# Optimization experiments

Hardware: AMD Instinct MI355X
Metric: run time of the kernel (lower is better)

Reference implementation:

```python
import jax, jax.numpy as jnp
import numpy as np

B = 4096
D = 64  # emb_dim, hardcoded in UserEmb/ItemEmb


def setup_inputs() -> dict:
    key = jax.random.key(0)
    ks = jax.random.split(key, 26)
    n = lambda k, shape, s=1.0: jax.random.normal(k, shape, dtype=jnp.float32) * s
    inp = {
        'user_emb': jax.random.randint(ks[0], (B, 4), 0, 6, dtype=jnp.int32),
        'item_emb': jax.random.randint(ks[1], (B, 10242), 0, 2, dtype=jnp.int32),
        'edge_emb': jnp.zeros((B,), dtype=jnp.int32),  # edges_emb has num_embeddings=1
        # UserEmb params
        'gender_tab': n(ks[2], (98, D)),
        'age_tab': n(ks[3], (7, D)),
        'occ_tab': n(ks[4], (21, D)),
        'area_tab': n(ks[5], (3402, D)),
        'user_W': n(ks[6], (4 * D, D), 0.05),  # stored [in,out]
        'user_b': n(ks[7], (D,), 0.05),
        # ItemEmb params
        'rate_tab': n(ks[8], (6, D)),
        'genre_W': n(ks[9], (25, D), 0.05),
        'director_W': n(ks[10], (2186, D), 0.02),
        'actor_W': n(ks[11], (8030, D), 0.01),
        'item_W': n(ks[12], (4 * D, D), 0.05),
        'item_b': n(ks[13], (D,), 0.05),
        # GLNFeat params (torch: randn * 0.5)
        'edges_tab': n(ks[14], (1, D)),
        'uu_w': n(ks[15], (D,), 0.5),
        'ui_w': n(ks[16], (D,), 0.5),
        'iu_w': n(ks[17], (D,), 0.5),
        'ii_w': n(ks[18], (D,), 0.5),
        'edge_W': n(ks[19], (D, D), 0.5),
        'uu_W1': n(ks[20], (D, D), 0.5),
        'ui_W1': n(ks[21], (D, D), 0.5),
        'iu_W1': n(ks[22], (D, D), 0.5),
        'ii_W1': n(ks[23], (D, D), 0.5),
    }
    return inp


def _lrelu(v):
    return jnp.where(v >= 0, v, 0.01 * v)  # nn.LeakyReLU default slope


def reference(user_emb, item_emb, edge_emb, gender_tab, age_tab, occ_tab, area_tab,
              user_W, user_b, rate_tab, genre_W, director_W, actor_W, item_W, item_b,
              edges_tab, uu_w, ui_w, iu_w, ii_w, edge_W, uu_W1, ui_W1, iu_W1, ii_W1):
    a = 0.12
    b = 0.12
    # UserEmb
    u_cat = jnp.concatenate([gender_tab[user_emb[:, 0]], age_tab[user_emb[:, 1]],
                             occ_tab[user_emb[:, 2]], area_tab[user_emb[:, 3]]], axis=1)
    x = (u_cat @ user_W + user_b) * a  # [B, D]
    # ItemEmb: multi-hot fields projected then mean-normalized by count
    genre = item_emb[:, 1:26].astype(jnp.float32)
    director = item_emb[:, 26:2212].astype(jnp.float32)
    actor = item_emb[:, 2212:10242].astype(jnp.float32)
    ge = (genre @ genre_W) / jnp.sum(genre, 1, keepdims=True)
    de = (director @ director_W) / jnp.sum(director, 1, keepdims=True)
    ae = (actor @ actor_W) / jnp.sum(actor, 1, keepdims=True)
    i_cat = jnp.concatenate([rate_tab[item_emb[:, 0]], ge, de, ae], axis=1)
    y = (i_cat @ item_W + item_b) * a  # [B, D]
    edge = edges_tab[edge_emb] * b  # [B, D]

    def outer_mm(u, v, M):
        # stop_gradient(outer(u, v) @ M) == u[:,None] * (v @ M), avoids [B,B]
        return jax.lax.stop_gradient(u[:, None] * (v @ M))

    xe = x * edge
    ye = y * edge
    x_xx = xe @ uu_w      # [B]
    x_xy_x = xe @ ui_w
    x_xy_y = ye @ ui_w
    t1 = outer_mm(x_xx, x_xx, x)
    t2 = outer_mm(x_xy_x, x_xy_y, y)
    x_buy = (_lrelu(t1 @ uu_W1) + _lrelu(t2 @ ui_W1)) / 2
    y_yy = ye @ ii_w
    y_yx_y = ye @ iu_w
    y_yx_x = xe @ iu_w
    t3 = outer_mm(y_yy, y_yy, y)
    t4 = outer_mm(y_yx_y, y_yx_x, x)
    y_buy = (_lrelu(t3 @ ii_W1) + _lrelu(t4 @ iu_W1)) / 2
    new = _lrelu(edge @ edge_W)
    return ((x_buy + x) / 2, (y_buy + y) / 2, (new + edge) / 2)
```

## Files before the change

### kernel.cpp

```cpp
#include <hip/hip_runtime.h>
#include <cstddef>

constexpr int BATCH = 4096;
constexpr int ITEM_COLS = 10242;

constexpr int R_GENDER = 0;
constexpr int R_AGE    = 98;
constexpr int R_OCC    = 105;
constexpr int R_AREA   = 126;
constexpr int R_RATE   = 3528;
constexpr int R_FU     = 3534;

__device__ const int CUM[10] = {0, 128, 1280, 2432, 3840, 5248, 6656, 8064, 9472, 10880};
__device__ const int DLT[9]  = {0, -104, -168, -224, -296, -368, -432, -504, -576};
__device__ const int LOG[9]  = {1, 130, 1287, 2436, 3846, 5256, 6659, 8069, 9479};
__device__ const int HIG[9]  = {26, 1223, 2380, 3774, 5184, 6595, 7997, 9407, 10818};
constexpr int FB2COLS = 10880;
constexpr int NSLICE  = 15;
__device__ const int TS_[16] = {0, 1, 7, 13, 19, 25, 31, 37, 43, 49, 55, 61, 67, 73, 79, 85};
__device__ const int TCH[85] = {
    0,
    1,1,1,1,1,1,1,1,1,
    2,2,2,2,2,2,2,2,2,
    3,3,3,3,3,3,3,3,3,3,3,
    4,4,4,4,4,4,4,4,4,4,4,
    5,5,5,5,5,5,5,5,5,5,5,
    6,6,6,6,6,6,6,6,6,6,6,
    7,7,7,7,7,7,7,7,7,7,7,
    8,8,8,8,8,8,8,8,8,8,8};

constexpr int NFUSEA = 884;
constexpr int NFUSET = FB2COLS / 64;

constexpr size_t OFF_FU  = 0;
constexpr size_t OFF_NEW = OFF_FU + (size_t)R_FU * 64;
constexpr size_t OFF_FBT = OFF_NEW + 64;
constexpr size_t OFF_X   = OFF_FBT + (size_t)64 * FB2COLS / 2;
constexpr size_t OFF_Y   = OFF_X + (size_t)BATCH * 64;
constexpr size_t OFF_P   = OFF_Y + (size_t)BATCH * 64;
constexpr size_t OFF_C   = OFF_P + (size_t)NSLICE * BATCH * 64;
constexpr size_t OFF_SP  = OFF_C + (size_t)NSLICE * BATCH;
constexpr size_t OFF_SC  = OFF_SP + 256ull * 256;

typedef __attribute__((ext_vector_type(8))) short bf16x8;
typedef __attribute__((ext_vector_type(4))) float f32x4;

__device__ __forceinline__ float lrelu(float v) { return v >= 0.0f ? v : 0.01f * v; }

__device__ __forceinline__ unsigned bf_rne_pair(float lo, float hi) {
    unsigned ul = __builtin_bit_cast(unsigned, lo);
    unsigned uh = __builtin_bit_cast(unsigned, hi);
    ul += 0x7fffu + ((ul >> 16) & 1u);
    uh += 0x7fffu + ((uh >> 16) & 1u);
    return (ul >> 16) | (uh & 0xffff0000u);
}

__global__ __launch_bounds__(256) void k_fuse(
        const float* __restrict__ gender_tab, const float* __restrict__ age_tab,
        const float* __restrict__ occ_tab, const float* __restrict__ area_tab,
        const float* __restrict__ user_W, const float* __restrict__ rate_tab,
        const float* __restrict__ item_W, const float* __restrict__ edges_tab,
        const float* __restrict__ edge_W, const float* __restrict__ genre_W,
        const float* __restrict__ director_W, const float* __restrict__ actor_W,
        float* __restrict__ Fu, float* __restrict__ NEWt, short* __restrict__ Fbt2) {
    const int t = threadIdx.x;
    const int n = t & 63;
    const int rb = __builtin_amdgcn_readfirstlane(t >> 6);
    __shared__ float T[64 * 65];
    const int blk = blockIdx.x;

    if (blk < NFUSEA) {
        int r = blk * 4 + rb;
        if (r > R_FU) return;
        if (r == R_FU) {
            float acc = 0.0f;
#pragma unroll
            for (int k = 0; k < 64; ++k)
                acc = fmaf(edges_tab[k] * 0.12f, edge_W[k * 64 + n], acc);
            NEWt[n] = lrelu(acc);
            return;
        }
        const float* src;
        const float* W;
        if (r < R_AGE)       { src = gender_tab + (size_t)r * 64;            W = user_W;            }
        else if (r < R_OCC)  { src = age_tab    + (size_t)(r - R_AGE) * 64;  W = user_W + 64 * 64;  }
        else if (r < R_AREA) { src = occ_tab    + (size_t)(r - R_OCC) * 64;  W = user_W + 128 * 64; }
        else if (r < R_RATE) { src = area_tab   + (size_t)(r - R_AREA) * 64; W = user_W + 192 * 64; }
        else                 { src = rate_tab   + (size_t)(r - R_RATE) * 64; W = item_W;            }
        float acc = 0.0f;
#pragma unroll
        for (int k = 0; k < 64; ++k)
            acc = fmaf(src[k], W[k * 64 + n], acc);
        Fu[(size_t)r * 64 + n] = acc;
        return;
    }

    const int g0 = (blk - NFUSEA) * 64;
    int ch = 0;
    while (g0 >= CUM[ch + 1]) ++ch;
    const int lo = LOG[ch], hi = HIG[ch], dl = DLT[ch];

    for (int rl = 0; rl < 16; ++rl) {
        int r = rl * 4 + rb;
        int g = g0 + r;
        float acc = 0.0f;
        if (g >= lo && g < hi) {
            int c = g + dl;
            const float* src;
            const float* W;
            if (c < 26)        { src = genre_W    + (size_t)(c - 1) * 64;    W = item_W + 64 * 64;  }
            else if (c < 2212) { src = director_W + (size_t)(c - 26) * 64;   W = item_W + 128 * 64; }
            else               { src = actor_W    + (size_t)(c - 2212) * 64; W = item_W + 192 * 64; }
#pragma unroll
            for (int k = 0; k < 64; ++k)
                acc = fmaf(src[k], W[k * 64 + n], acc);
        }
        T[r * 65 + n] = acc;
    }
    __syncthreads();
    int n2 = t >> 2, sg = t & 3;
    unsigned dw[8];
#pragma unroll
    for (int d = 0; d < 8; ++d)
        dw[d] = bf_rne_pair(T[(sg * 16 + 2 * d) * 65 + n2], T[(sg * 16 + 2 * d + 1) * 65 + n2]);
    uint4* dst = (uint4*)(Fbt2 + (size_t)n2 * FB2COLS + g0 + sg * 16);
    dst[0] = make_uint4(dw[0], dw[1], dw[2], dw[3]);
    dst[1] = make_uint4(dw[4], dw[5], dw[6], dw[7]);
}

__global__ __launch_bounds__(256) void k_item(const int* __restrict__ item,
                                              const short* __restrict__ Fbt2,
                                              float* __restrict__ P, float* __restrict__ C) {
    const int slc = blockIdx.y;
    const int kt0 = TS_[slc], kt1 = TS_[slc + 1];
    const int m0 = blockIdx.x * 64;
    const int t = threadIdx.x;
    const int lane = t & 63;
    const int w = __builtin_amdgcn_readfirstlane(t >> 6);
    const int q = lane >> 4, r16 = lane & 15;

    __shared__ short As[64 * 136];
    __shared__ short Bs[64 * 136];

    f32x4 acc[5];
#pragma unroll
    for (int s = 0; s < 5; ++s) acc[s] = (f32x4){0.f, 0.f, 0.f, 0.f};

    const short o = (r16 == 0) ? (short)0x3f80 : (short)0;
    const bf16x8 ones = {o, o, o, o, o, o, o, o};

    int2 av[16];
    uint4 bv[4];
    const int nB = t >> 2, pt = t & 3;
    const int* arow = item + (size_t)(m0 + w) * ITEM_COLS + 2 * lane;
    const short* brow = Fbt2 + (size_t)nB * FB2COLS;

    auto fetch = [&](int kt) {
        const int ch = TCH[kt];
        const int c0 = kt * 128 + DLT[ch];
        if (c0 + 128 <= ITEM_COLS) {
            const int* ap = arow + c0;
#pragma unroll
            for (int it = 0; it < 16; ++it)
                av[it] = *(const int2*)(ap + (size_t)it * 4 * ITEM_COLS);
        } else {
            const bool ok = (c0 + 2 * lane) <= (ITEM_COLS - 2);
            const int ccl = ok ? (c0 + 2 * lane) : (ITEM_COLS - 2);
            const int* ap = item + (size_t)(m0 + w) * ITEM_COLS + ccl;
#pragma unroll
            for (int it = 0; it < 16; ++it) {
                int2 v = *(const int2*)(ap + (size_t)it * 4 * ITEM_COLS);
                av[it].x = ok ? v.x : 0;
                av[it].y = ok ? v.y : 0;
            }
        }
        const short* bp = brow + kt * 128;
#pragma unroll
        for (int p = 0; p < 4; ++p)
            bv[p] = *(const uint4*)(bp + (p * 4 + pt) * 8);
    };

    fetch(kt0);
    for (int kt = kt0; kt < kt1; ++kt) {
#pragma unroll
        for (int it = 0; it < 16; ++it) {
            unsigned d = (av[it].x ? 0x3f80u : 0u) | (av[it].y ? 0x3f800000u : 0u);
            *(unsigned*)(As + (it * 4 + w) * 136 + 2 * lane) = d;
        }
#pragma unroll
        for (int p = 0; p < 4; ++p)
            *(uint4*)(Bs + nB * 136 + (p * 4 + pt) * 8) = bv[p];
        if (kt + 1 < kt1) fetch(kt + 1);
        asm volatile("s_waitcnt lgkmcnt(0)\n\ts_barrier" ::: "memory");

        const int ch = TCH[kt];
        const int g0 = kt * 128;
        const int lo = LOG[ch] - g0, hi = HIG[ch] - g0;
        const bool edge = (lo > 0) || (hi < 128);
#pragma unroll
        for (int ks = 0; ks < 4; ++ks) {
            bf16x8 a = *(const bf16x8*)(As + (w * 16 + r16) * 136 + ks * 32 + q * 8);
            bf16x8 ov = ones;
            if (edge) {
#pragma unroll
                for (int j = 0; j < 8; ++j) {
                    int kk = ks * 32 + q * 8 + j;
                    ov[j] = (kk >= lo && kk < hi) ? o : (short)0;
                }
            }
#pragma unroll
            for (int s = 0; s < 4; ++s) {
                bf16x8 b = *(const bf16x8*)(Bs + (s * 16 + r16) * 136 + ks * 32 + q * 8);
                acc[s] = __builtin_amdgcn_mfma_f32_16x16x32_bf16(a, b, acc[s], 0, 0, 0);
            }
            acc[4] = __builtin_amdgcn_mfma_f32_16x16x32_bf16(a, ov, acc[4], 0, 0, 0);
        }
        asm volatile("s_barrier" ::: "memory");
    }
    const size_t pb = (size_t)slc * BATCH + m0 + w * 16 + q * 4;
#pragma unroll
    for (int reg = 0; reg < 4; ++reg) {
        float* pr = P + (pb + reg) * 64 + r16;
        pr[0] = acc[0][reg];
        pr[16] = acc[1][reg];
        pr[32] = acc[2][reg];
        pr[48] = acc[3][reg];
    }
    if (r16 == 0) {
#pragma unroll
        for (int reg = 0; reg < 4; ++reg)
            C[(size_t)slc * BATCH + m0 + w * 16 + q * 4 + reg] = acc[4][reg];
    }
}

__device__ __forceinline__ float wred(float v) {
#pragma unroll
    for (int m = 1; m < 64; m <<= 1) v += __shfl_xor(v, m, 64);
    return v;
}

__global__ __launch_bounds__(256) void k_mid(const int* __restrict__ item, const int* __restrict__ edge_emb,
                                             const int* __restrict__ user_emb,
                                             const float* __restrict__ Fu, const float* __restrict__ user_b,
                                             const float* __restrict__ P, const float* __restrict__ C,
                                             const float* __restrict__ item_b, const float* __restrict__ edges_tab,
                                             const float* __restrict__ uu_w, const float* __restrict__ ui_w,
                                             const float* __restrict__ iu_w, const float* __restrict__ ii_w,
                                             float* __restrict__ X, float* __restrict__ Y,
                                             float* __restrict__ SC, float* __restrict__ SP) {
    const int t = threadIdx.x;
    const int n = t & 63;
    const int wv = __builtin_amdgcn_readfirstlane(t >> 6);
    const float uuw = uu_w[n], uiw = ui_w[n], iuw = iu_w[n], iiw = ii_w[n];
    const float ib = item_b[n], ub = user_b[n];
    const size_t cs = (size_t)BATCH * 64;
    float s1 = 0.0f, s2 = 0.0f, s3 = 0.0f, s4 = 0.0f;

    for (int i = 0; i < 4; ++i) {
        int b = blockIdx.x * 16 + wv * 4 + i;
        const int* ue = user_emb + (size_t)b * 4;
        float x = (Fu[(size_t)(R_GENDER + ue[0]) * 64 + n]
                 + Fu[(size_t)(R_AGE    + ue[1]) * 64 + n]
                 + Fu[(size_t)(R_OCC    + ue[2]) * 64 + n]
                 + Fu[(size_t)(R_AREA   + ue[3]) * 64 + n] + ub) * 0.12f;
        X[(size_t)b * 64 + n] = x;
        int ri = item[(size_t)b * ITEM_COLS];
        size_t base = (size_t)b * 64 + n;
        float sg = P[base];
        float cg = C[b];
        float sd = 0.0f, cd = 0.0f, sa = 0.0f, ca = 0.0f;
#pragma unroll
        for (int s5 = 1; s5 < 4; ++s5) { sd += P[base + s5 * cs]; cd += C[s5 * BATCH + b]; }
#pragma unroll
        for (int s5 = 4; s5 < NSLICE; ++s5) { sa += P[base + s5 * cs]; ca += C[s5 * BATCH + b]; }
        float y = (Fu[(size_t)(R_RATE + ri) * 64 + n] + sg / cg + sd / cd + sa / ca + ib) * 0.12f;
        Y[(size_t)b * 64 + n] = y;
        float e = edges_tab[(size_t)edge_emb[b] * 64 + n] * 0.12f;
        float xe = x * e, ye = y * e;
        float r1 = wred(xe * uuw);
        float r2 = wred(xe * uiw);
        float r3 = wred(xe * iuw);
        float r4 = wred(ye * uiw);
        float r5 = wred(ye * iiw);
        float r6 = wred(ye * iuw);
        if (n == 0) {
            SC[b] = r1; SC[BATCH + b] = r2; SC[2 * BATCH + b] = r5; SC[3 * BATCH + b] = r6;
        }
        s1 = fmaf(r1, x, s1);
        s2 = fmaf(r4, y, s2);
        s3 = fmaf(r5, y, s3);
        s4 = fmaf(r3, x, s4);
    }
    __shared__ float sp[4][4][64];
    sp[wv][0][n] = s1; sp[wv][1][n] = s2; sp[wv][2][n] = s3; sp[wv][3][n] = s4;
    __syncthreads();
    int i2 = t >> 6;
    float v = sp[0][i2][n] + sp[1][i2][n] + sp[2][i2][n] + sp[3][i2][n];
    SP[(size_t)blockIdx.x * 256 + t] = v;
}

__global__ __launch_bounds__(256) void k_out(const float* __restrict__ X, const float* __restrict__ Y,
                                             const float* __restrict__ SC, const float* __restrict__ SP,
                                             const float* __restrict__ NEWt, const float* __restrict__ edges_tab,
                                             const int* __restrict__ edge_emb,
                                             const float* __restrict__ uu_W1, const float* __restrict__ ui_W1,
                                             const float* __restrict__ iu_W1, const float* __restrict__ ii_W1,
                                             float* __restrict__ out) {
    const int t = threadIdx.x;
    const int i = t >> 6, n = t & 63;
    float s = 0.0f;
    for (int wb = 0; wb < 256; ++wb) s += SP[(size_t)wb * 256 + t];
    __shared__ float sl2[4][64];
    sl2[i][n] = s;
    __syncthreads();
    const float* W1 = (i == 0) ? uu_W1 : (i == 1) ? ui_W1 : (i == 2) ? ii_W1 : iu_W1;
    float p = 0.0f;
#pragma unroll
    for (int k = 0; k < 64; ++k) p = fmaf(sl2[i][k], W1[k * 64 + n], p);
    __shared__ float pbs[4][64];
    pbs[i][n] = p;
    __syncthreads();
    const float p1 = pbs[0][n], p2 = pbs[1][n], p3 = pbs[2][n], p4 = pbs[3][n];
    const float nw = NEWt[n];
#pragma unroll
    for (int j = 0; j < 8; ++j) {
        int b = blockIdx.x * 32 + j * 4 + i;
        float xx = SC[b], xyx = SC[BATCH + b], yy = SC[2 * BATCH + b], yxy = SC[3 * BATCH + b];
        float x = X[(size_t)b * 64 + n], y = Y[(size_t)b * 64 + n];
        float o1 = ((lrelu(xx * p1) + lrelu(xyx * p2)) * 0.5f + x) * 0.5f;
        float o2 = ((lrelu(yy * p3) + lrelu(yxy * p4)) * 0.5f + y) * 0.5f;
        float e = edges_tab[(size_t)edge_emb[b] * 64 + n] * 0.12f;
        float o3 = (nw + e) * 0.5f;
        out[(size_t)b * 64 + n] = o1;
        out[((size_t)BATCH + b) * 64 + n] = o2;
        out[((size_t)2 * BATCH + b) * 64 + n] = o3;
    }
}

extern "C" void kernel_launch(void* const* d_in, const int* in_sizes, int n_in,
                              void* d_out, int out_size, void* d_ws, size_t ws_size,
                              hipStream_t stream) {
    (void)in_sizes; (void)n_in; (void)out_size; (void)ws_size;
    const int*   user_emb   = (const int*)  d_in[0];
    const int*   item_emb   = (const int*)  d_in[1];
    const int*   edge_emb   = (const int*)  d_in[2];
    const float* gender_tab = (const float*)d_in[3];
    const float* age_tab    = (const float*)d_in[4];
    const float* occ_tab    = (const float*)d_in[5];
    const float* area_tab   = (const float*)d_in[6];
    const float* user_W     = (const float*)d_in[7];
    const float* user_b     = (const float*)d_in[8];
    const float* rate_tab   = (const float*)d_in[9];
    const float* genre_W    = (const float*)d_in[10];
    const float* director_W = (const float*)d_in[11];
    const float* actor_W    = (const float*)d_in[12];
    const float* item_W     = (const float*)d_in[13];
    const float* item_b     = (const float*)d_in[14];
    const float* edges_tab  = (const float*)d_in[15];
    const float* uu_w       = (const float*)d_in[16];
    const float* ui_w       = (const float*)d_in[17];
    const float* iu_w       = (const float*)d_in[18];
    const float* ii_w       = (const float*)d_in[19];
    const float* edge_W     = (const float*)d_in[20];
    const float* uu_W1      = (const float*)d_in[21];
    const float* ui_W1      = (const float*)d_in[22];
    const float* iu_W1      = (const float*)d_in[23];
    const float* ii_W1      = (const float*)d_in[24];

    float* ws   = (float*)d_ws;
    float* Fu   = ws + OFF_FU;
    float* NEWt = ws + OFF_NEW;
    short* Fbt2 = (short*)(ws + OFF_FBT);
    float* X    = ws + OFF_X;
    float* Y    = ws + OFF_Y;
    float* P    = ws + OFF_P;
    float* C    = ws + OFF_C;
    float* SP   = ws + OFF_SP;
    float* SC   = ws + OFF_SC;
    float* out  = (float*)d_out;

    hipLaunchKernelGGL(k_fuse, dim3(NFUSEA + NFUSET), dim3(256), 0, stream,
                       gender_tab, age_tab, occ_tab, area_tab, user_W, rate_tab,
                       item_W, edges_tab, edge_W, genre_W, director_W, actor_W,
                       Fu, NEWt, Fbt2);
    hipLaunchKernelGGL(k_item, dim3(BATCH / 64, NSLICE), dim3(256), 0, stream, item_emb, Fbt2, P, C);
    hipLaunchKernelGGL(k_mid, dim3(BATCH / 16), dim3(256), 0, stream,
                       item_emb, edge_emb, user_emb, Fu, user_b, P, C, item_b, edges_tab,
                       uu_w, ui_w, iu_w, ii_w, X, Y, SC, SP);
    hipLaunchKernelGGL(k_out, dim3(BATCH / 32), dim3(256), 0, stream,
                       X, Y, SC, SP, NEWt, edges_tab, edge_emb,
                       uu_W1, ui_W1, iu_W1, ii_W1, out);
}
```

Measured before the change: 366.1 us.

## Bit-pack multi-hot item matrix and pre-swizzle B into MFMA fragment order

Adds packer blocks to the fuse kernel that ballot the int32 multi-hot item columns into 64-bit masks per row, with column-validity masking folded in. The fused weight matrix is written directly in MFMA operand fragment order. The item GEMM kernel then drops its LDS staging and barriers, expanding mask bits into bf16 A fragments in registers and loading B fragments straight from global memory. The intent is to cut the 168MB int32 read and the LDS traffic out of the GEMM. The cost is an extra mask-building pass, which still reads the full item matrix, plus uncoalesced B loads that rely on cache.

```diff
diff --git a/kernel.cpp b/kernel.cpp
--- a/kernel.cpp
+++ b/kernel.cpp
@@ -16,26 +16,41 @@
 __device__ const int LOG[9]  = {1, 130, 1287, 2436, 3846, 5256, 6659, 8069, 9479};
 __device__ const int HIG[9]  = {26, 1223, 2380, 3774, 5184, 6595, 7997, 9407, 10818};
 constexpr int FB2COLS = 10880;
+constexpr int NTILE   = 85;
 constexpr int NSLICE  = 15;
 __device__ const int TS_[16] = {0, 1, 7, 13, 19, 25, 31, 37, 43, 49, 55, 61, 67, 73, 79, 85};
-__device__ const int TCH[85] = {
-    0,
-    1,1,1,1,1,1,1,1,1,
-    2,2,2,2,2,2,2,2,2,
-    3,3,3,3,3,3,3,3,3,3,3,
-    4,4,4,4,4,4,4,4,4,4,4,
-    5,5,5,5,5,5,5,5,5,5,5,
-    6,6,6,6,6,6,6,6,6,6,6,
-    7,7,7,7,7,7,7,7,7,7,7,
-    8,8,8,8,8,8,8,8,8,8,8};
 
 constexpr int NFUSEA = 884;
 constexpr int NFUSET = FB2COLS / 64;
+constexpr int NPACK  = 1024;
+
+struct PackTab { unsigned long long vm[NFUSET]; int c0[NFUSET]; };
+constexpr PackTab make_packtab() {
+    PackTab p{};
+    const int CUMc[10] = {0, 128, 1280, 2432, 3840, 5248, 6656, 8064, 9472, 10880};
+    const int DLTc[9]  = {0, -104, -168, -224, -296, -368, -432, -504, -576};
+    const int LOGc[9]  = {1, 130, 1287, 2436, 3846, 5256, 6659, 8069, 9479};
+    const int HIGc[9]  = {26, 1223, 2380, 3774, 5184, 6595, 7997, 9407, 10818};
+    for (int wq = 0; wq < NFUSET; ++wq) {
+        int g0 = wq * 64;
+        int ch = 0;
+        while (g0 >= CUMc[ch + 1]) ++ch;
+        int lo = LOGc[ch] - g0; lo = lo < 0 ? 0 : lo;
+        int hi = HIGc[ch] - g0; hi = hi < 0 ? 0 : (hi > 64 ? 64 : hi);
+        unsigned long long hm = (hi >= 64) ? ~0ull : ((1ull << hi) - 1ull);
+        unsigned long long lm = (lo <= 0) ? 0ull : ((1ull << lo) - 1ull);
+        p.vm[wq] = hm & ~lm;
+        p.c0[wq] = g0 + DLTc[ch];
+    }
+    return p;
+}
+__device__ constexpr PackTab PT = make_packtab();
 
 constexpr size_t OFF_FU  = 0;
 constexpr size_t OFF_NEW = OFF_FU + (size_t)R_FU * 64;
 constexpr size_t OFF_FBT = OFF_NEW + 64;
-constexpr size_t OFF_X   = OFF_FBT + (size_t)64 * FB2COLS / 2;
+constexpr size_t OFF_MSK = OFF_FBT + (size_t)64 * FB2COLS / 2;
+constexpr size_t OFF_X   = OFF_MSK + (size_t)BATCH * (FB2COLS / 64) * 2;
 constexpr size_t OFF_Y   = OFF_X + (size_t)BATCH * 64;
 constexpr size_t OFF_P   = OFF_Y + (size_t)BATCH * 64;
 constexpr size_t OFF_C   = OFF_P + (size_t)NSLICE * BATCH * 64;
@@ -44,6 +59,7 @@
 
 typedef __attribute__((ext_vector_type(8))) short bf16x8;
 typedef __attribute__((ext_vector_type(4))) float f32x4;
+typedef __attribute__((ext_vector_type(4))) unsigned u32x4;
 
 __device__ __forceinline__ float lrelu(float v) { return v >= 0.0f ? v : 0.01f * v; }
 
@@ -62,12 +78,31 @@
         const float* __restrict__ item_W, const float* __restrict__ edges_tab,
         const float* __restrict__ edge_W, const float* __restrict__ genre_W,
         const float* __restrict__ director_W, const float* __restrict__ actor_W,
-        float* __restrict__ Fu, float* __restrict__ NEWt, short* __restrict__ Fbt2) {
+        const int* __restrict__ item,
+        float* __restrict__ Fu, float* __restrict__ NEWt, short* __restrict__ B2s,
+        unsigned long long* __restrict__ M64) {
     const int t = threadIdx.x;
+    const int blk = blockIdx.x;
+
+    if (blk >= NFUSEA + NFUSET) {
+        const int w = __builtin_amdgcn_readfirstlane(t >> 6);
+        const int lane = t & 63;
+        const int m = (blk - (NFUSEA + NFUSET)) * 4 + w;
+        const int* row = item + (size_t)m * ITEM_COLS;
+        unsigned long long* dst = M64 + (size_t)m * (FB2COLS / 64);
+#pragma unroll 2
+        for (int wq = 0; wq < FB2COLS / 64; ++wq) {
+            int c = PT.c0[wq] + lane;
+            c = c > (ITEM_COLS - 1) ? (ITEM_COLS - 1) : c;
+            unsigned long long b = __ballot(row[c] != 0) & PT.vm[wq];
+            if (lane == 0) dst[wq] = b;
+        }
+        return;
+    }
+
     const int n = t & 63;
     const int rb = __builtin_amdgcn_readfirstlane(t >> 6);
     __shared__ float T[64 * 65];
-    const int blk = blockIdx.x;
 
     if (blk < NFUSEA) {
         int r = blk * 4 + rb;
@@ -123,13 +158,18 @@
 #pragma unroll
     for (int d = 0; d < 8; ++d)
         dw[d] = bf_rne_pair(T[(sg * 16 + 2 * d) * 65 + n2], T[(sg * 16 + 2 * d + 1) * 65 + n2]);
-    uint4* dst = (uint4*)(Fbt2 + (size_t)n2 * FB2COLS + g0 + sg * 16);
-    dst[0] = make_uint4(dw[0], dw[1], dw[2], dw[3]);
-    dst[1] = make_uint4(dw[4], dw[5], dw[6], dw[7]);
-}
-
-__global__ __launch_bounds__(256) void k_item(const int* __restrict__ item,
-                                              const short* __restrict__ Fbt2,
+    const int kt = g0 >> 7;
+    const int kl = (g0 & 127) + sg * 16;
+    const int ks = kl >> 5;
+    const int qa = (kl >> 3) & 3;
+    const int s = n2 >> 4, r16b = n2 & 15;
+    const size_t slot0 = (size_t)kt * 1024 + ks * 256 + s * 64 + qa * 16 + r16b;
+    *(uint4*)(B2s + slot0 * 8)        = make_uint4(dw[0], dw[1], dw[2], dw[3]);
+    *(uint4*)(B2s + (slot0 + 16) * 8) = make_uint4(dw[4], dw[5], dw[6], dw[7]);
+}
+
+__global__ __launch_bounds__(256) void k_item(const unsigned long long* __restrict__ M64,
+                                              const short* __restrict__ B2s,
                                               float* __restrict__ P, float* __restrict__ C) {
     const int slc = blockIdx.y;
     const int kt0 = TS_[slc], kt1 = TS_[slc + 1];
@@ -138,9 +178,7 @@
     const int lane = t & 63;
     const int w = __builtin_amdgcn_readfirstlane(t >> 6);
     const int q = lane >> 4, r16 = lane & 15;
-
-    __shared__ short As[64 * 136];
-    __shared__ short Bs[64 * 136];
+    const int m = m0 + w * 16 + r16;
 
     f32x4 acc[5];
 #pragma unroll
@@ -149,73 +187,28 @@
     const short o = (r16 == 0) ? (short)0x3f80 : (short)0;
     const bf16x8 ones = {o, o, o, o, o, o, o, o};
 
-    int2 av[16];
-    uint4 bv[4];
-    const int nB = t >> 2, pt = t & 3;
-    const int* arow = item + (size_t)(m0 + w) * ITEM_COLS + 2 * lane;
-    const short* brow = Fbt2 + (size_t)nB * FB2COLS;
-
-    auto fetch = [&](int kt) {
-        const int ch = TCH[kt];
-        const int c0 = kt * 128 + DLT[ch];
-        if (c0 + 128 <= ITEM_COLS) {
-            const int* ap = arow + c0;
-#pragma unroll
-            for (int it = 0; it < 16; ++it)
-                av[it] = *(const int2*)(ap + (size_t)it * 4 * ITEM_COLS);
-        } else {
-            const bool ok = (c0 + 2 * lane) <= (ITEM_COLS - 2);
-            const int ccl = ok ? (c0 + 2 * lane) : (ITEM_COLS - 2);
-            const int* ap = item + (size_t)(m0 + w) * ITEM_COLS + ccl;
-#pragma unroll
-            for (int it = 0; it < 16; ++it) {
-                int2 v = *(const int2*)(ap + (size_t)it * 4 * ITEM_COLS);
-                av[it].x = ok ? v.x : 0;
-                av[it].y = ok ? v.y : 0;
-            }
-        }
-        const short* bp = brow + kt * 128;
-#pragma unroll
-        for (int p = 0; p < 4; ++p)
-            bv[p] = *(const uint4*)(bp + (p * 4 + pt) * 8);
-    };
-
-    fetch(kt0);
+    const u32x4* mrow = (const u32x4*)(M64 + (size_t)m * (FB2COLS / 64));
+    const bf16x8* b2 = (const bf16x8*)B2s;
+
     for (int kt = kt0; kt < kt1; ++kt) {
-#pragma unroll
-        for (int it = 0; it < 16; ++it) {
-            unsigned d = (av[it].x ? 0x3f80u : 0u) | (av[it].y ? 0x3f800000u : 0u);
-            *(unsigned*)(As + (it * 4 + w) * 136 + 2 * lane) = d;
-        }
-#pragma unroll
-        for (int p = 0; p < 4; ++p)
-            *(uint4*)(Bs + nB * 136 + (p * 4 + pt) * 8) = bv[p];
-        if (kt + 1 < kt1) fetch(kt + 1);
-        asm volatile("s_waitcnt lgkmcnt(0)\n\ts_barrier" ::: "memory");
-
-        const int ch = TCH[kt];
-        const int g0 = kt * 128;
-        const int lo = LOG[ch] - g0, hi = HIG[ch] - g0;
-        const bool edge = (lo > 0) || (hi < 128);
+        u32x4 mv = mrow[kt];
+        const bf16x8* bp = b2 + (size_t)kt * 1024 + lane;
 #pragma unroll
         for (int ks = 0; ks < 4; ++ks) {
-            bf16x8 a = *(const bf16x8*)(As + (w * 16 + r16) * 136 + ks * 32 + q * 8);
-            bf16x8 ov = ones;
-            if (edge) {
-#pragma unroll
-                for (int j = 0; j < 8; ++j) {
-                    int kk = ks * 32 + q * 8 + j;
-                    ov[j] = (kk >= lo && kk < hi) ? o : (short)0;
-                }
-            }
+            unsigned by = (mv[ks] >> (q * 8)) & 0xffu;
+            u32x4 ev;
+#pragma unroll
+            for (int p2 = 0; p2 < 4; ++p2)
+                ev[p2] = (((by >> (2 * p2)) & 1u) ? 0x3f80u : 0u)
+                       | (((by >> (2 * p2 + 1)) & 1u) ? 0x3f800000u : 0u);
+            bf16x8 a = __builtin_bit_cast(bf16x8, ev);
 #pragma unroll
             for (int s = 0; s < 4; ++s) {
-                bf16x8 b = *(const bf16x8*)(Bs + (s * 16 + r16) * 136 + ks * 32 + q * 8);
+                bf16x8 b = bp[ks * 256 + s * 64];
                 acc[s] = __builtin_amdgcn_mfma_f32_16x16x32_bf16(a, b, acc[s], 0, 0, 0);
             }
-            acc[4] = __builtin_amdgcn_mfma_f32_16x16x32_bf16(a, ov, acc[4], 0, 0, 0);
-        }
-        asm volatile("s_barrier" ::: "memory");
+            acc[4] = __builtin_amdgcn_mfma_f32_16x16x32_bf16(a, ones, acc[4], 0, 0, 0);
+        }
     }
     const size_t pb = (size_t)slc * BATCH + m0 + w * 16 + q * 4;
 #pragma unroll
@@ -370,7 +363,8 @@
     float* ws   = (float*)d_ws;
     float* Fu   = ws + OFF_FU;
     float* NEWt = ws + OFF_NEW;
-    short* Fbt2 = (short*)(ws + OFF_FBT);
+    short* B2s  = (short*)(ws + OFF_FBT);
+    unsigned long long* M64 = (unsigned long long*)(ws + OFF_MSK);
     float* X    = ws + OFF_X;
     float* Y    = ws + OFF_Y;
     float* P    = ws + OFF_P;
@@ -379,11 +373,11 @@
     float* SC   = ws + OFF_SC;
     float* out  = (float*)d_out;
 
-    hipLaunchKernelGGL(k_fuse, dim3(NFUSEA + NFUSET), dim3(256), 0, stream,
+    hipLaunchKernelGGL(k_fuse, dim3(NFUSEA + NFUSET + NPACK), dim3(256), 0, stream,
                        gender_tab, age_tab, occ_tab, area_tab, user_W, rate_tab,
                        item_W, edges_tab, edge_W, genre_W, director_W, actor_W,
-                       Fu, NEWt, Fbt2);
-    hipLaunchKernelGGL(k_item, dim3(BATCH / 64, NSLICE), dim3(256), 0, stream, item_emb, Fbt2, P, C);
+                       item_emb, Fu, NEWt, B2s, M64);
+    hipLaunchKernelGGL(k_item, dim3(BATCH / 64, NSLICE), dim3(256), 0, stream, M64, B2s, P, C);
     hipLaunchKernelGGL(k_mid, dim3(BATCH / 16), dim3(256), 0, stream,
                        item_emb, edge_emb, user_emb, Fu, user_b, P, C, item_b, edges_tab,
                        uu_w, ui_w, iu_w, ii_w, X, Y, SC, SP);
```

Result: slower. 387.2 us (+5.8%).
